# Kernel tuning notes

Hardware: AMD Instinct MI355X
Metric: run time of the kernel (lower is better)

The kernel has to match this reference:

```python
import jax, jax.numpy as jnp
import numpy as np

# dims (must match input_specs / init_kwargs)
T, B_SZ, K, OBS_LAST = 512, 8, 128, 2
OBS_DIM = K * OBS_LAST          # 256
N_ACTIONS = 64
N_UNITS, N_FEAT = 256, 8
D_INNER = N_UNITS * N_FEAT      # 2048
H, N_STATE = 16, 64             # p_heads, state_size
P = D_INNER // H                # headdim = 128


def setup_inputs() -> dict:
    key = jax.random.key(0)
    ks = jax.random.split(key, 12)
    s = lambda fan_in: 1.0 / np.sqrt(fan_in)
    return {
        "obs": jax.random.normal(ks[0], (T, B_SZ, K, OBS_LAST), jnp.float32),
        # input projection obs_dim -> d_inner
        "W_in": jax.random.normal(ks[1], (OBS_DIM, D_INNER), jnp.float32) * s(OBS_DIM),
        "b_in": jnp.zeros((D_INNER,), jnp.float32),
        # SSD cell params (Mamba2-style)
        "A_log": jnp.log(jnp.linspace(1.0, 16.0, H).astype(jnp.float32)),
        "dt_bias": jnp.full((H,), -2.0, jnp.float32),
        "W_dt": jax.random.normal(ks[2], (D_INNER, H), jnp.float32) * s(D_INNER),
        "W_B": jax.random.normal(ks[3], (D_INNER, H * N_STATE), jnp.float32) * s(D_INNER),
        "W_C": jax.random.normal(ks[4], (D_INNER, H * N_STATE), jnp.float32) * s(D_INNER),
        # SSD output projection d_inner -> n_units
        "W_yo": jax.random.normal(ks[5], (D_INNER, N_UNITS), jnp.float32) * s(D_INNER),
        "b_yo": jnp.zeros((N_UNITS,), jnp.float32),
        # policy head n_units -> n_actions
        "W_head": jax.random.normal(ks[6], (N_UNITS, N_ACTIONS), jnp.float32) * s(N_UNITS),
        "b_head": jnp.zeros((N_ACTIONS,), jnp.float32),
    }


def _ssd_scan(x, A_log, dt_bias, W_dt, W_B, W_C):
    # x: (T, B, D_INNER) -> y: (T, B, D_INNER) via selective state-space scan
    t, b, _ = x.shape
    dt = jax.nn.softplus(jnp.einsum("tbd,dh->tbh", x, W_dt) + dt_bias)   # (T,B,H)
    Bm = jnp.einsum("tbd,dm->tbm", x, W_B).reshape(t, b, H, N_STATE)      # (T,B,H,N)
    Cm = jnp.einsum("tbd,dm->tbm", x, W_C).reshape(t, b, H, N_STATE)      # (T,B,H,N)
    xh = x.reshape(t, b, H, P)                                            # (T,B,H,P)
    decay = jnp.exp(-jnp.exp(A_log)[None, None, :] * dt)                  # (T,B,H)

    def step(h, inp):
        dec_t, dt_t, B_t, C_t, x_t = inp
        # h: (B,H,P,N); rank-1 input update per head
        h = dec_t[:, :, None, None] * h + dt_t[:, :, None, None] * jnp.einsum(
            "bhp,bhn->bhpn", x_t, B_t)
        y = jnp.einsum("bhpn,bhn->bhp", h, C_t)                           # (B,H,P)
        return h, y

    h0 = jnp.zeros((b, H, P, N_STATE), x.dtype)
    _, ys = jax.lax.scan(step, h0, (decay, dt, Bm, Cm, xh))
    return ys.reshape(t, b, D_INNER)


def reference(obs, W_in, b_in, A_log, dt_bias, W_dt, W_B, W_C, W_yo, b_yo, W_head, b_head):
    t, b = obs.shape[0], obs.shape[1]
    flat = obs.reshape(t * b, -1)                                 # (t*B, obs_dim)
    x = jax.nn.relu(flat @ W_in + b_in).reshape(t, b, D_INNER)     # (t,B,d_inner)
    y = _ssd_scan(x, A_log, dt_bias, W_dt, W_B, W_C)               # (t,B,d_inner)
    hid = jnp.einsum("tbd,du->tbu", y, W_yo) + b_yo                # (t,B,n_units)
    z = jax.nn.relu(hid).reshape(t * b, N_UNITS)
    logits = z @ W_head + b_head
    return logits.reshape(t, b, N_ACTIONS)
```

## Files before the change

kernel.cpp:

```cpp
#include <hip/hip_runtime.h>
#include <cstdint>
#include <cstddef>

typedef unsigned short u16;
typedef __attribute__((ext_vector_type(8))) __bf16 bf16x8;
typedef __attribute__((ext_vector_type(4))) float floatx4;

#define T_DIM   512
#define B_SZ    8
#define ROWS    4096
#define OBS_D   256
#define D_IN    2048
#define NHEAD   16
#define NSTATE  64
#define PDIM    128
#define NUNITS  256
#define NACT    64
#define NSEG    4
#define SEGT    128
#define SLOT    (B_SZ * NHEAD * PDIM * NSTATE)
#define BCSTR   2176
#define BCN     2048

__host__ __device__ __forceinline__ float bf2f(u16 u) {
    union { uint32_t i; float f; } v; v.i = ((uint32_t)u) << 16; return v.f;
}
__host__ __device__ __forceinline__ u16 f2bf(float f) {
    union { float f; uint32_t i; } v; v.f = f;
    uint32_t r = v.i + 0x7FFFu + ((v.i >> 16) & 1u);
    return (u16)(r >> 16);
}

__device__ __forceinline__ void glds16(const u16* g, u16* l) {
    __builtin_amdgcn_global_load_lds(
        (__attribute__((address_space(1))) void*)g,
        (__attribute__((address_space(3))) void*)l, 16, 0, 0);
}

__global__ __launch_bounds__(256) void ActorAgent_27625229647898_kernel(
        float* __restrict__ out, int n, float v) {
    for (int i = blockIdx.x * 256 + threadIdx.x; i < n; i += gridDim.x * 256)
        out[i] = v;
}

__global__ __launch_bounds__(256) void prep(const float* __restrict__ obs,
                                            const float* __restrict__ W_dt,
                                            const float* __restrict__ W_in,
                                            const float* __restrict__ W_B,
                                            const float* __restrict__ W_C,
                                            const float* __restrict__ W_yo,
                                            const float* __restrict__ W_head,
                                            u16* __restrict__ obsb,
                                            u16* __restrict__ WinT, u16* __restrict__ WBCT,
                                            u16* __restrict__ WdtT,
                                            u16* __restrict__ WyoT, u16* __restrict__ WheadT) {
    int bid = blockIdx.x;
    if (bid < 160) {
        const int NOBS = ROWS * OBS_D;
        const int NDT  = D_IN * NHEAD;
        for (int i = bid * 256 + threadIdx.x; i < NOBS + NDT; i += 160 * 256) {
            if (i < NOBS) obsb[i] = f2bf(obs[i]);
            else {
                int j = i - NOBS;
                int k = j >> 4, n = j & 15;
                WdtT[n * D_IN + k] = f2bf(W_dt[j]);
            }
        }
        return;
    }
    bid -= 160;
    const float* src; u16* dst; int R, C, bx, by;
    if (bid < 512)       { src = W_in;   dst = WinT;   R = 256;  C = 2048; bx = bid & 63; by = bid >> 6; }
    else if (bid < 2560) { int i = bid - 512;  src = W_B;  dst = WBCT; R = 2048; C = 1024; bx = i & 31; by = i >> 5; }
    else if (bid < 4608) { int i = bid - 2560; src = W_C;  dst = WBCT + (size_t)1024 * 2048; R = 2048; C = 1024; bx = i & 31; by = i >> 5; }
    else if (bid < 5120) { int i = bid - 4608; src = W_yo; dst = WyoT; R = 2048; C = 256;  bx = i & 7;  by = i >> 3; }
    else                 { int i = bid - 5120; src = W_head; dst = WheadT; R = 256; C = 64; bx = i & 1; by = i >> 1; }
    __shared__ float t[32][33];
    int c0 = bx * 32, r0 = by * 32;
    int tx = threadIdx.x & 31, ty = threadIdx.x >> 5;
#pragma unroll
    for (int i = 0; i < 32; i += 8)
        t[ty + i][tx] = src[(size_t)(r0 + ty + i) * C + c0 + tx];
    __syncthreads();
#pragma unroll
    for (int i = 0; i < 32; i += 8)
        dst[(size_t)(c0 + ty + i) * R + r0 + tx] = f2bf(t[tx][ty + i]);
}

template <int ACT, int OUT_BF16, int HAS_BIAS>
__global__ __launch_bounds__(256) void gemm_bt128(const u16* __restrict__ A,
                                                  const u16* __restrict__ BT,
                                                  const float* __restrict__ bias,
                                                  void* __restrict__ Cout,
                                                  int M, int N, int K, int ldc) {
    __shared__ __align__(16) u16 sA[2][128 * 64];
    __shared__ __align__(16) u16 sB[2][128 * 64];
    const int tid  = threadIdx.x;
    const int wave = tid >> 6, lane = tid & 63;
    const int quad = lane >> 4, lr = lane & 15;
    const int wm = wave & 1, wn = wave >> 1;
    const int m0 = blockIdx.x * 128, n0 = blockIdx.y * 128;
    const int r0 = wave * 32 + (lane >> 3);
    const int kel = (((lane & 7) ^ ((lane >> 3) & 7))) * 8;
    const int rsw = lr & 7;

    floatx4 acc[4][4];
#pragma unroll
    for (int i = 0; i < 4; i++)
#pragma unroll
        for (int j = 0; j < 4; j++)
#pragma unroll
            for (int r = 0; r < 4; r++) acc[i][j][r] = 0.f;

    const u16* apg = A + (size_t)(m0 + r0) * K + kel;
    const u16* bpg = BT + (size_t)(n0 + r0) * K + kel;
    const int ntk = K >> 6;

#define STAGE128(t, sb) do {                                                   \
        int kk_ = (t) << 6;                                                    \
        _Pragma("unroll")                                                      \
        for (int g = 0; g < 4; ++g) {                                          \
            glds16(apg + (size_t)(g * 8) * K + kk_,                            \
                   &sA[sb][(wave * 32 + g * 8) * 64]);                         \
            glds16(bpg + (size_t)(g * 8) * K + kk_,                            \
                   &sB[sb][(wave * 32 + g * 8) * 64]);                         \
        }                                                                      \
    } while (0)

    STAGE128(0, 0);
    for (int t = 0; t < ntk; ++t) {
        const int s = t & 1;
        asm volatile("s_waitcnt vmcnt(0)" ::: "memory");
        __builtin_amdgcn_s_barrier();
        asm volatile("" ::: "memory");
        if (t + 1 < ntk) STAGE128(t + 1, s ^ 1);
#pragma unroll
        for (int ks = 0; ks < 2; ++ks) {
            bf16x8 af[4], bfr[4];
#pragma unroll
            for (int i = 0; i < 4; i++)
                af[i] = *(const bf16x8*)&sA[s][(wm * 64 + i * 16 + lr) * 64 + ((ks * 4 + quad) ^ rsw) * 8];
#pragma unroll
            for (int j = 0; j < 4; j++)
                bfr[j] = *(const bf16x8*)&sB[s][(wn * 64 + j * 16 + lr) * 64 + ((ks * 4 + quad) ^ rsw) * 8];
#pragma unroll
            for (int i = 0; i < 4; i++)
#pragma unroll
                for (int j = 0; j < 4; j++)
                    acc[i][j] = __builtin_amdgcn_mfma_f32_16x16x32_bf16(af[i], bfr[j], acc[i][j], 0, 0, 0);
        }
        asm volatile("" ::: "memory");
    }
#undef STAGE128
#pragma unroll
    for (int j = 0; j < 4; j++) {
        int col = n0 + wn * 64 + j * 16 + lr;
        float bvv = HAS_BIAS ? bias[col] : 0.f;
#pragma unroll
        for (int i = 0; i < 4; i++) {
#pragma unroll
            for (int r = 0; r < 4; r++) {
                int row = m0 + wm * 64 + i * 16 + quad * 4 + r;
                float v = acc[i][j][r] + bvv;
                if (ACT) v = fmaxf(v, 0.f);
                if (OUT_BF16) ((u16*)Cout)[(size_t)row * ldc + col] = f2bf(v);
                else          ((float*)Cout)[(size_t)row * ldc + col] = v;
            }
        }
    }
}

template <int ACT, int OUT_BF16>
__global__ __launch_bounds__(256) void gemm_bt64(const u16* __restrict__ A,
                                                 const u16* __restrict__ BT,
                                                 const float* __restrict__ bias,
                                                 void* __restrict__ Cout,
                                                 int M, int N, int K) {
    __shared__ __align__(16) u16 sA[4][64 * 64];
    __shared__ __align__(16) u16 sB[4][64 * 64];
    const int tid  = threadIdx.x;
    const int wave = tid >> 6, lane = tid & 63;
    const int quad = lane >> 4, lr = lane & 15;
    const int m0 = blockIdx.x * 64, n0 = blockIdx.y * 64;
    const int srl = lane >> 3;
    const int sc = (((lane & 7) ^ ((lane >> 3) & 7))) * 8;
    const int rsw = lr & 7;

    floatx4 acc[4];
#pragma unroll
    for (int i = 0; i < 4; i++)
#pragma unroll
        for (int j = 0; j < 4; j++) acc[i][j] = 0.f;

    const u16* apg = A + (size_t)(m0 + wave * 16 + srl) * K + sc;
    const u16* bpg = BT + (size_t)(n0 + wave * 16 + srl) * K + sc;
    const int ntk = K >> 6;

#define STAGE64(t, sb) do {                                            \
        int kk_ = (t) << 6;                                            \
        glds16(apg + kk_,                 &sA[sb][(wave * 16) * 64]);  \
        glds16(apg + (size_t)8 * K + kk_, &sA[sb][(wave * 16 + 8) * 64]);\
        glds16(bpg + kk_,                 &sB[sb][(wave * 16) * 64]);  \
        glds16(bpg + (size_t)8 * K + kk_, &sB[sb][(wave * 16 + 8) * 64]);\
    } while (0)

    STAGE64(0, 0);
    STAGE64(1, 1);
    for (int t = 0; t < ntk; ++t) {
        const int s = t & 3;
        if (t + 1 < ntk) {
            asm volatile("s_waitcnt vmcnt(4)" ::: "memory");
        } else {
            asm volatile("s_waitcnt vmcnt(0)" ::: "memory");
        }
        __builtin_amdgcn_s_barrier();
        asm volatile("" ::: "memory");
        __builtin_amdgcn_s_setprio(1);
#pragma unroll
        for (int ks = 0; ks < 2; ++ks) {
            bf16x8 af = *(const bf16x8*)&sA[s][(wave * 16 + lr) * 64 + ((ks * 4 + quad) ^ rsw) * 8];
#pragma unroll
            for (int nt = 0; nt < 4; nt++) {
                bf16x8 bf = *(const bf16x8*)&sB[s][(nt * 16 + lr) * 64 + ((ks * 4 + quad) ^ rsw) * 8];
                acc[nt] = __builtin_amdgcn_mfma_f32_16x16x32_bf16(af, bf, acc[nt], 0, 0, 0);
            }
        }
        __builtin_amdgcn_s_setprio(0);
        asm volatile("" ::: "memory");
        if (t + 2 < ntk) STAGE64(t + 2, (t + 2) & 3);
    }
#undef STAGE64
#pragma unroll
    for (int nt = 0; nt < 4; nt++) {
        int col = n0 + nt * 16 + lr;
        float bvv = bias ? bias[col] : 0.f;
#pragma unroll
        for (int r = 0; r < 4; r++) {
            int row = m0 + wave * 16 + quad * 4 + r;
            float v = acc[nt][r] + bvv;
            if (ACT) v = fmaxf(v, 0.f);
            if (OUT_BF16) ((u16*)Cout)[(size_t)row * N + col] = f2bf(v);
            else          ((float*)Cout)[(size_t)row * N + col] = v;
        }
    }
}

__global__ __launch_bounds__(512) void dtdecay(const u16* __restrict__ xb,
                                               const u16* __restrict__ WdtT,
                                               const float* __restrict__ dt_bias,
                                               const float* __restrict__ A_log,
                                               float* __restrict__ dtv,
                                               float* __restrict__ decayv) {
    __shared__ __align__(16) u16 sw[NHEAD * D_IN];
    const int tid = threadIdx.x;
#pragma unroll
    for (int i = 0; i < 8; ++i) {
        int idx = (tid + i * 512) * 8;
        *(uint4*)&sw[idx] = *(const uint4*)(WdtT + idx);
    }
    __syncthreads();
    const int wave = tid >> 6, lane = tid & 63;
    const int q = lane >> 4, lr = lane & 15;
    const int row0 = blockIdx.x * 16 + wave * 2;
    const u16* xp0 = xb + (size_t)row0 * D_IN;
    const u16* xp1 = xb + (size_t)(row0 + 1) * D_IN;
    float acc0[4] = {0.f, 0.f, 0.f, 0.f};
    float acc1[4] = {0.f, 0.f, 0.f, 0.f};
#pragma unroll 4
    for (int k0 = 0; k0 < 16; ++k0) {
        const int kk = k0 * 128 + lr * 8;
        uint4 xv0 = *(const uint4*)(xp0 + kk);
        uint4 xv1 = *(const uint4*)(xp1 + kk);
        const u16* xu0 = (const u16*)&xv0;
        const u16* xu1 = (const u16*)&xv1;
        float xf0[8], xf1[8];
#pragma unroll
        for (int j = 0; j < 8; ++j) { xf0[j] = bf2f(xu0[j]); xf1[j] = bf2f(xu1[j]); }
#pragma unroll
        for (int j = 0; j < 4; ++j) {
            uint4 wv = *(const uint4*)&sw[(q * 4 + j) * D_IN + kk];
            const u16* wu = (const u16*)&wv;
#pragma unroll
            for (int jj = 0; jj < 8; ++jj) {
                float wf = bf2f(wu[jj]);
                acc0[j] = fmaf(xf0[jj], wf, acc0[j]);
                acc1[j] = fmaf(xf1[jj], wf, acc1[j]);
            }
        }
    }
#pragma unroll
    for (int m = 1; m <= 8; m <<= 1)
#pragma unroll
        for (int j = 0; j < 4; ++j) {
            acc0[j] += __shfl_xor(acc0[j], m);
            acc1[j] += __shfl_xor(acc1[j], m);
        }
    if (lr == 0) {
#pragma unroll
        for (int j = 0; j < 4; ++j) {
            int h = q * 4 + j;
            float ae = expf(A_log[h]);
            float z0 = acc0[j] + dt_bias[h];
            float sp0 = (z0 > 20.f) ? z0 : log1pf(expf(z0));
            float z1 = acc1[j] + dt_bias[h];
            float sp1 = (z1 > 20.f) ? z1 : log1pf(expf(z1));
            dtv[row0 * NHEAD + h] = sp0;
            decayv[row0 * NHEAD + h] = expf(-ae * sp0);
            dtv[(row0 + 1) * NHEAD + h] = sp1;
            decayv[(row0 + 1) * NHEAD + h] = expf(-ae * sp1);
        }
    }
}

__global__ __launch_bounds__(256) void seg_state(const u16* __restrict__ xw,
                                                 const u16* __restrict__ BCm,
                                                 const float* __restrict__ dtv,
                                                 const float* __restrict__ decayv,
                                                 float* __restrict__ Hbuf) {
    const int blk = blockIdx.x;
    const int seg = blk >> 7;
    const int b   = (blk >> 4) & 7;
    const int h   = blk & 15;
    const int tid = threadIdx.x;
    const int pgrp = tid >> 3;
    const int oct  = tid & 7;

    __shared__ __align__(16) u16 sx[SEGT][PDIM];
    __shared__ __align__(16) u16 sbm[SEGT][NSTATE];
    __shared__ float sw[SEGT];
    __shared__ float sdt[SEGT];
    __shared__ float sdec[SEGT];
    __shared__ float sP[32];

    const int t0 = seg * SEGT;

#pragma unroll
    for (int k = 0; k < 8; ++k) {
        int idx = tid + k * 256;
        int t = idx >> 4, c = (idx & 15) * 8;
        int r = (t0 + t) * B_SZ + b;
        *(uint4*)&sx[t][c] = *(const uint4*)(xw + (size_t)r * D_IN + h * PDIM + c);
    }
#pragma unroll
    for (int k = 0; k < 4; ++k) {
        int idx = tid + k * 256;
        int t = idx >> 3, c = (idx & 7) * 8;
        int r = (t0 + t) * B_SZ + b;
        *(uint4*)&sbm[t][c] = *(const uint4*)(BCm + (size_t)r * BCSTR + h * NSTATE + c);
    }
    if (tid < SEGT)            sdt[tid] = dtv[((t0 + tid) * B_SZ + b) * NHEAD + h];
    else if (tid < 2 * SEGT)   sdec[tid - SEGT] = decayv[((t0 + tid - SEGT) * B_SZ + b) * NHEAD + h];
    __syncthreads();

    if (tid < 32) {
        float p = 1.f;
        for (int i = 3; i >= 0; --i) {
            int t = tid * 4 + i;
            sw[t] = sdt[t] * p;
            p *= sdec[t];
        }
        sP[tid] = p;
    }
    __syncthreads();
    if (tid == 0) {
        float suf = 1.f;
        for (int q = 31; q >= 0; --q) { float tmp = sP[q]; sP[q] = suf; suf *= tmp; }
    }
    __syncthreads();
    if (tid < 32) {
        float m = sP[tid];
        for (int i = 0; i < 4; ++i) sw[tid * 4 + i] *= m;
    }
    __syncthreads();

    float acc[4][8];
#pragma unroll
    for (int i = 0; i < 4; i++)
#pragma unroll
        for (int j = 0; j < 8; j++) acc[i][j] = 0.f;

    for (int t = 0; t < SEGT; ++t) {
        float w = sw[t];
        const u16* xp = &sx[t][pgrp * 4];
        const u16* bp = &sbm[t][oct * 8];
        float xv[4], bv[8];
#pragma unroll
        for (int i = 0; i < 4; i++) xv[i] = w * bf2f(xp[i]);
#pragma unroll
        for (int j = 0; j < 8; j++) bv[j] = bf2f(bp[j]);
#pragma unroll
        for (int i = 0; i < 4; i++)
#pragma unroll
            for (int j = 0; j < 8; j++)
                acc[i][j] = fmaf(xv[i], bv[j], acc[i][j]);
    }

    float* base = Hbuf + (size_t)seg * SLOT +
                  (((size_t)b * NHEAD + h) * PDIM + pgrp * 4) * NSTATE + oct * 8;
#pragma unroll
    for (int i = 0; i < 4; i++) {
        *(float4*)(base + (size_t)i * NSTATE)     = make_float4(acc[i][0], acc[i][1], acc[i][2], acc[i][3]);
        *(float4*)(base + (size_t)i * NSTATE + 4) = make_float4(acc[i][4], acc[i][5], acc[i][6], acc[i][7]);
    }
}

__global__ __launch_bounds__(256) void seg_prefix(const float* __restrict__ Hbuf,
                                                  const float* __restrict__ decayv,
                                                  u16* __restrict__ Hbf) {
    const int blk = blockIdx.x;
    const int b  = blk >> 6;
    const int h  = (blk >> 2) & 15;
    const int ec = blk & 3;
    const int tid = threadIdx.x;

    __shared__ float sA[NSEG];

    if (tid < 64 * (NSEG - 2)) {
        int s = 1 + (tid >> 6);
        int i = tid & 63;
        int t = s * SEGT + i * 2;
        float p = decayv[(t * B_SZ + b) * NHEAD + h] *
                  decayv[((t + 1) * B_SZ + b) * NHEAD + h];
        p *= __shfl_xor(p, 1);
        p *= __shfl_xor(p, 2);
        p *= __shfl_xor(p, 4);
        p *= __shfl_xor(p, 8);
        p *= __shfl_xor(p, 16);
        p *= __shfl_xor(p, 32);
        if (i == 0) sA[s] = p;
    }
    __syncthreads();

    const size_t base = (((size_t)b * NHEAD + h) * PDIM * NSTATE) + (size_t)ec * 2048 + tid * 8;
    float4 P0 = *(const float4*)(Hbuf + base);
    float4 P1 = *(const float4*)(Hbuf + base + 4);
    u16 pk[8];
    pk[0] = f2bf(P0.x); pk[1] = f2bf(P0.y); pk[2] = f2bf(P0.z); pk[3] = f2bf(P0.w);
    pk[4] = f2bf(P1.x); pk[5] = f2bf(P1.y); pk[6] = f2bf(P1.z); pk[7] = f2bf(P1.w);
    *(uint4*)(Hbf + base) = *(const uint4*)pk;
#pragma unroll
    for (int s = 1; s <= NSEG - 2; ++s) {
        float a = sA[s];
        const float* slot = Hbuf + (size_t)s * SLOT + base;
        float4 h0 = *(const float4*)(slot);
        float4 h1 = *(const float4*)(slot + 4);
        P0.x = fmaf(a, P0.x, h0.x); P0.y = fmaf(a, P0.y, h0.y);
        P0.z = fmaf(a, P0.z, h0.z); P0.w = fmaf(a, P0.w, h0.w);
        P1.x = fmaf(a, P1.x, h1.x); P1.y = fmaf(a, P1.y, h1.y);
        P1.z = fmaf(a, P1.z, h1.z); P1.w = fmaf(a, P1.w, h1.w);
        pk[0] = f2bf(P0.x); pk[1] = f2bf(P0.y); pk[2] = f2bf(P0.z); pk[3] = f2bf(P0.w);
        pk[4] = f2bf(P1.x); pk[5] = f2bf(P1.y); pk[6] = f2bf(P1.z); pk[7] = f2bf(P1.w);
        *(uint4*)(Hbf + (size_t)s * SLOT + base) = *(const uint4*)pk;
    }
}

__global__ __launch_bounds__(256) void chunk_scan(const u16* __restrict__ BCm,
                                                  const float* __restrict__ dtv,
                                                  const float* __restrict__ decayv,
                                                  const u16* __restrict__ Hbf,
                                                  u16* __restrict__ xb) {
    __shared__ __align__(16) u16 sB_[128][68];
    __shared__ __align__(16) u16 sC_[128][68];
    __shared__ __align__(16) u16 sS[128][132];
    __shared__ __align__(16) u16 sXT[128][36];
    __shared__ float sdt[SEGT], sL[SEGT], sEL[SEGT], stmp[32];

    const int blk = blockIdx.x;
    const int seg = blk >> 7, b = (blk >> 4) & 7, h = blk & 15;
    const int tid = threadIdx.x;
    const int wave = tid >> 6, lane = tid & 63;
    const int quad = lane >> 4, lr = lane & 15;
    const int wm = wave & 1, wn = wave >> 1;
    const int t0 = seg * SEGT;

#pragma unroll
    for (int it = 0; it < 4; ++it) {
        int idx = tid + it * 256;
        int t = idx >> 3, c = (idx & 7) * 8;
        int r = (t0 + t) * B_SZ + b;
        *(uint4*)&sB_[t][c] = *(const uint4*)(BCm + (size_t)r * BCSTR + h * NSTATE + c);
        *(uint4*)&sC_[t][c] = *(const uint4*)(BCm + (size_t)r * BCSTR + 1024 + h * NSTATE + c);
    }
    if (tid < SEGT) sdt[tid] = dtv[((t0 + tid) * B_SZ + b) * NHEAD + h];
    else if (tid < 2 * SEGT) {
        int t = tid - SEGT;
        sL[t] = __logf(fmaxf(decayv[((t0 + t) * B_SZ + b) * NHEAD + h], 1e-30f));
    }
    __syncthreads();
    if (tid < 32) {
        float s = 0.f, v[4];
#pragma unroll
        for (int i = 0; i < 4; ++i) { s += sL[tid * 4 + i]; v[i] = s; }
        stmp[tid] = s;
#pragma unroll
        for (int i = 0; i < 4; ++i) sL[tid * 4 + i] = v[i];
    }
    __syncthreads();
    if (tid == 0) {
        float run = 0.f;
        for (int q = 0; q < 32; ++q) { float c2 = stmp[q]; stmp[q] = run; run += c2; }
    }
    __syncthreads();
    if (tid < 32) {
        float off = stmp[tid];
#pragma unroll
        for (int i = 0; i < 4; ++i) sL[tid * 4 + i] += off;
    }
    __syncthreads();
    if (tid < SEGT) sEL[tid] = __expf(sL[tid]);

    floatx4 accS[4][4];
#pragma unroll
    for (int i = 0; i < 4; i++)
#pragma unroll
        for (int j = 0; j < 4; j++)
#pragma unroll
            for (int r = 0; r < 4; r++) accS[i][j][r] = 0.f;
#pragma unroll
    for (int k0 = 0; k0 < 64; k0 += 32) {
        bf16x8 af[4], bfr[4];
#pragma unroll
        for (int i = 0; i < 4; i++)
            af[i] = *(const bf16x8*)&sB_[wm * 64 + i * 16 + lr][k0 + quad * 8];
#pragma unroll
        for (int j = 0; j < 4; j++)
            bfr[j] = *(const bf16x8*)&sC_[wn * 64 + j * 16 + lr][k0 + quad * 8];
#pragma unroll
        for (int i = 0; i < 4; i++)
#pragma unroll
            for (int j = 0; j < 4; j++)
                accS[i][j] = __builtin_amdgcn_mfma_f32_16x16x32_bf16(af[i], bfr[j], accS[i][j], 0, 0, 0);
    }
#pragma unroll
    for (int j = 0; j < 4; j++) {
        int tt = wn * 64 + j * 16 + lr;
        float Lt = sL[tt];
#pragma unroll
        for (int i = 0; i < 4; i++) {
#pragma unroll
            for (int r = 0; r < 4; r++) {
                int tp = wm * 64 + i * 16 + quad * 4 + r;
                float v = 0.f;
                if (tp <= tt) v = accS[i][j][r] * sdt[tp] * __expf(Lt - sL[tp]);
                sS[tt][tp] = f2bf(v);
            }
        }
    }

    floatx4 acc[4][4];
#pragma unroll
    for (int i = 0; i < 4; i++)
#pragma unroll
        for (int j = 0; j < 4; j++)
#pragma unroll
            for (int r = 0; r < 4; r++) acc[i][j][r] = 0.f;
    __syncthreads();
    if (seg > 0) {
        const u16* hbase = Hbf + (size_t)(seg - 1) * SLOT + (((size_t)b * NHEAD + h) * PDIM) * NSTATE;
#pragma unroll
        for (int k0 = 0; k0 < 64; k0 += 32) {
            bf16x8 af[4], bfr[4];
#pragma unroll
            for (int i = 0; i < 4; i++)
                af[i] = *(const bf16x8*)&sC_[wm * 64 + i * 16 + lr][k0 + quad * 8];
#pragma unroll
            for (int j = 0; j < 4; j++)
                bfr[j] = *(const bf16x8*)(hbase + (size_t)(wn * 64 + j * 16 + lr) * NSTATE + k0 + quad * 8);
#pragma unroll
            for (int i = 0; i < 4; i++)
#pragma unroll
                for (int j = 0; j < 4; j++)
                    acc[i][j] = __builtin_amdgcn_mfma_f32_16x16x32_bf16(af[i], bfr[j], acc[i][j], 0, 0, 0);
        }
#pragma unroll
        for (int i = 0; i < 4; i++) {
#pragma unroll
            for (int r = 0; r < 4; r++) {
                float el = sEL[wm * 64 + i * 16 + quad * 4 + r];
#pragma unroll
                for (int j = 0; j < 4; j++) acc[i][j][r] *= el;
            }
        }
    }

    const int px = tid & 127, koh = (tid >> 7) * 16;
    for (int kc = 0; kc < 128; kc += 32) {
        u16 xv[16];
#pragma unroll
        for (int j2 = 0; j2 < 16; ++j2) {
            int tp = kc + koh + j2;
            xv[j2] = xb[(size_t)((t0 + tp) * B_SZ + b) * D_IN + h * PDIM + px];
        }
        __syncthreads();
        *(uint4*)&sXT[px][koh]     = *(const uint4*)&xv[0];
        *(uint4*)&sXT[px][koh + 8] = *(const uint4*)&xv[8];
        __syncthreads();
        bf16x8 af[4], bfr[4];
#pragma unroll
        for (int i = 0; i < 4; i++)
            af[i] = *(const bf16x8*)&sS[wm * 64 + i * 16 + lr][kc + quad * 8];
#pragma unroll
        for (int j = 0; j < 4; j++)
            bfr[j] = *(const bf16x8*)&sXT[wn * 64 + j * 16 + lr][quad * 8];
#pragma unroll
        for (int i = 0; i < 4; i++)
#pragma unroll
            for (int j = 0; j < 4; j++)
                acc[i][j] = __builtin_amdgcn_mfma_f32_16x16x32_bf16(af[i], bfr[j], acc[i][j], 0, 0, 0);
    }

#pragma unroll
    for (int j = 0; j < 4; j++) {
        int p = wn * 64 + j * 16 + lr;
#pragma unroll
        for (int i = 0; i < 4; i++) {
#pragma unroll
            for (int r = 0; r < 4; r++) {
                int t = wm * 64 + i * 16 + quad * 4 + r;
                xb[(size_t)((t0 + t) * B_SZ + b) * D_IN + h * PDIM + p] = f2bf(acc[i][j][r]);
            }
        }
    }
}

extern "C" void kernel_launch(void* const* d_in, const int* in_sizes, int n_in,
                              void* d_out, int out_size, void* d_ws, size_t ws_size,
                              hipStream_t stream) {
    const float* obs     = (const float*)d_in[0];
    const float* W_in    = (const float*)d_in[1];
    const float* b_in    = (const float*)d_in[2];
    const float* A_log   = (const float*)d_in[3];
    const float* dt_bias = (const float*)d_in[4];
    const float* W_dt    = (const float*)d_in[5];
    const float* W_B     = (const float*)d_in[6];
    const float* W_C     = (const float*)d_in[7];
    const float* W_yo    = (const float*)d_in[8];
    const float* b_yo    = (const float*)d_in[9];
    const float* W_head  = (const float*)d_in[10];
    const float* b_head  = (const float*)d_in[11];

    char* ws = (char*)d_ws;
    size_t o = 0;
    u16*   xb     = (u16*)(ws + o);   o += (size_t)ROWS * D_IN * 2;
    u16*   BCm    = (u16*)(ws + o);   o += (size_t)ROWS * BCSTR * 2;
    float* dtv    = (float*)(ws + o); o += (size_t)ROWS * NHEAD * 4;
    float* decayv = (float*)(ws + o); o += (size_t)ROWS * NHEAD * 4;
    u16*   zb     = (u16*)(ws + o);   o += (size_t)ROWS * NUNITS * 2;
    float* Hseg   = (float*)(ws + o); o += (size_t)(NSEG - 1) * SLOT * 4;
    u16*   Hbf    = (u16*)(ws + o);   o += (size_t)(NSEG - 1) * SLOT * 2;
    u16*   obsb   = (u16*)(ws + o);   o += (size_t)ROWS * OBS_D * 2;
    u16*   WinT   = (u16*)(ws + o);   o += (size_t)D_IN * OBS_D * 2;
    u16*   WBCT   = (u16*)(ws + o);   o += (size_t)BCN * D_IN * 2;
    u16*   WdtT   = (u16*)(ws + o);   o += (size_t)NHEAD * D_IN * 2;
    u16*   WyoT   = (u16*)(ws + o);   o += (size_t)NUNITS * D_IN * 2;
    u16*   WheadT = (u16*)(ws + o);   o += (size_t)NACT * NUNITS * 2;

    ActorAgent_27625229647898_kernel<<<dim3(1), 256, 0, stream>>>((float*)d_out, 0, 0.f);

    prep<<<dim3(160 + 5136), 256, 0, stream>>>(obs, W_dt, W_in, W_B, W_C, W_yo, W_head,
                                               obsb, WinT, WBCT, WdtT, WyoT, WheadT);

    gemm_bt128<1, 1, 1><<<dim3(32, 16), 256, 0, stream>>>(obsb, WinT, b_in, xb, ROWS, D_IN, OBS_D, D_IN);
    dtdecay<<<dim3(256), 512, 0, stream>>>(xb, WdtT, dt_bias, A_log, dtv, decayv);
    gemm_bt128<0, 1, 0><<<dim3(32, 16), 256, 0, stream>>>(xb, WBCT, (const float*)nullptr, BCm, ROWS, BCN, D_IN, BCSTR);
    seg_state<<<dim3((NSEG - 1) * 128), 256, 0, stream>>>(xb, BCm, dtv, decayv, Hseg);
    seg_prefix<<<dim3(512), 256, 0, stream>>>(Hseg, decayv, Hbf);
    chunk_scan<<<dim3(NSEG * 128), 256, 0, stream>>>(BCm, dtv, decayv, Hbf, xb);
    gemm_bt64<1, 1><<<dim3(64, 4), 256, 0, stream>>>(xb, WyoT, b_yo, zb, ROWS, NUNITS, D_IN);
    gemm_bt64<0, 0><<<dim3(64, 1), 256, 0, stream>>>(zb, WheadT, b_head, (float*)d_out, ROWS, NACT, NUNITS);
}
```

Baseline: 232.7 us.

## Move segment-state outer product to MFMA and deepen GEMM K-tile to 128

```diff
diff --git a/kernel.cpp b/kernel.cpp
--- a/kernel.cpp
+++ b/kernel.cpp
@@ -36,6 +36,9 @@
         (__attribute__((address_space(1))) void*)g,
         (__attribute__((address_space(3))) void*)l, 16, 0, 0);
 }
+
+#define LBAR() do { asm volatile("s_waitcnt lgkmcnt(0)" ::: "memory"); \
+                    __builtin_amdgcn_s_barrier(); } while (0)
 
 __global__ __launch_bounds__(256) void ActorAgent_27625229647898_kernel(
         float* __restrict__ out, int n, float v) {
@@ -176,15 +179,14 @@
                                                  const float* __restrict__ bias,
                                                  void* __restrict__ Cout,
                                                  int M, int N, int K) {
-    __shared__ __align__(16) u16 sA[4][64 * 64];
-    __shared__ __align__(16) u16 sB[4][64 * 64];
+    __shared__ __align__(16) u16 sA[2][64 * 128];
+    __shared__ __align__(16) u16 sB[2][64 * 128];
     const int tid  = threadIdx.x;
     const int wave = tid >> 6, lane = tid & 63;
     const int quad = lane >> 4, lr = lane & 15;
     const int m0 = blockIdx.x * 64, n0 = blockIdx.y * 64;
-    const int srl = lane >> 3;
-    const int sc = (((lane & 7) ^ ((lane >> 3) & 7))) * 8;
-    const int rsw = lr & 7;
+    const int rl = lane >> 4;
+    const int cl = lane & 15;
 
     floatx4 acc[4];
 #pragma unroll
@@ -192,42 +194,44 @@
 #pragma unroll
         for (int j = 0; j < 4; j++) acc[i][j] = 0.f;
 
-    const u16* apg = A + (size_t)(m0 + wave * 16 + srl) * K + sc;
-    const u16* bpg = BT + (size_t)(n0 + wave * 16 + srl) * K + sc;
-    const int ntk = K >> 6;
-
-#define STAGE64(t, sb) do {                                            \
-        int kk_ = (t) << 6;                                            \
-        glds16(apg + kk_,                 &sA[sb][(wave * 16) * 64]);  \
-        glds16(apg + (size_t)8 * K + kk_, &sA[sb][(wave * 16 + 8) * 64]);\
-        glds16(bpg + kk_,                 &sB[sb][(wave * 16) * 64]);  \
-        glds16(bpg + (size_t)8 * K + kk_, &sB[sb][(wave * 16 + 8) * 64]);\
+    size_t aoff[4], boff[4];
+#pragma unroll
+    for (int g = 0; g < 4; ++g) {
+        int ro = g * 4 + rl;
+        int ch = cl ^ ro;
+        aoff[g] = (size_t)(m0 + wave * 16 + ro) * K + (size_t)ch * 8;
+        boff[g] = (size_t)(n0 + wave * 16 + ro) * K + (size_t)ch * 8;
+    }
+    const int ntk = K >> 7;
+
+#define STAGE64(t, sb) do {                                                    \
+        int kk_ = (t) << 7;                                                    \
+        _Pragma("unroll")                                                      \
+        for (int g = 0; g < 4; ++g) {                                          \
+            glds16(A + aoff[g] + kk_,  &sA[sb][(wave * 16 + g * 4) * 128]);    \
+            glds16(BT + boff[g] + kk_, &sB[sb][(wave * 16 + g * 4) * 128]);    \
+        }                                                                      \
     } while (0)
 
     STAGE64(0, 0);
-    STAGE64(1, 1);
     for (int t = 0; t < ntk; ++t) {
-        const int s = t & 3;
-        if (t + 1 < ntk) {
-            asm volatile("s_waitcnt vmcnt(4)" ::: "memory");
-        } else {
-            asm volatile("s_waitcnt vmcnt(0)" ::: "memory");
-        }
+        const int s = t & 1;
+        asm volatile("s_waitcnt vmcnt(0)" ::: "memory");
         __builtin_amdgcn_s_barrier();
         asm volatile("" ::: "memory");
+        if (t + 1 < ntk) STAGE64(t + 1, s ^ 1);
         __builtin_amdgcn_s_setprio(1);
 #pragma unroll
-        for (int ks = 0; ks < 2; ++ks) {
-            bf16x8 af = *(const bf16x8*)&sA[s][(wave * 16 + lr) * 64 + ((ks * 4 + quad) ^ rsw) * 8];
+        for (int ks = 0; ks < 4; ++ks) {
+            bf16x8 af = *(const bf16x8*)&sA[s][(wave * 16 + lr) * 128 + ((ks * 4 + quad) ^ lr) * 8];
 #pragma unroll
             for (int nt = 0; nt < 4; nt++) {
-                bf16x8 bf = *(const bf16x8*)&sB[s][(nt * 16 + lr) * 64 + ((ks * 4 + quad) ^ rsw) * 8];
+                bf16x8 bf = *(const bf16x8*)&sB[s][(nt * 16 + lr) * 128 + ((ks * 4 + quad) ^ lr) * 8];
                 acc[nt] = __builtin_amdgcn_mfma_f32_16x16x32_bf16(af, bf, acc[nt], 0, 0, 0);
             }
         }
         __builtin_amdgcn_s_setprio(0);
         asm volatile("" ::: "memory");
-        if (t + 2 < ntk) STAGE64(t + 2, (t + 2) & 3);
     }
 #undef STAGE64
 #pragma unroll
@@ -322,85 +326,114 @@
     const int b   = (blk >> 4) & 7;
     const int h   = blk & 15;
     const int tid = threadIdx.x;
-    const int pgrp = tid >> 3;
-    const int oct  = tid & 7;
-
-    __shared__ __align__(16) u16 sx[SEGT][PDIM];
-    __shared__ __align__(16) u16 sbm[SEGT][NSTATE];
-    __shared__ float sw[SEGT];
-    __shared__ float sdt[SEGT];
-    __shared__ float sdec[SEGT];
-    __shared__ float sP[32];
+    const int wave = tid >> 6, lane = tid & 63;
+    const int quad = lane >> 4, lr = lane & 15;
+    const int wm = wave & 1, wn = wave >> 1;
+
+    __shared__ __align__(16) u16 sxw[PDIM][SEGT + 4];
+    __shared__ __align__(16) u16 sbT[NSTATE][SEGT + 6];
+    __shared__ float sw_[SEGT], sdt[SEGT], sdec[SEGT], sP[32];
 
     const int t0 = seg * SEGT;
 
+    uint4 xv4[8];
 #pragma unroll
     for (int k = 0; k < 8; ++k) {
         int idx = tid + k * 256;
         int t = idx >> 4, c = (idx & 15) * 8;
         int r = (t0 + t) * B_SZ + b;
-        *(uint4*)&sx[t][c] = *(const uint4*)(xw + (size_t)r * D_IN + h * PDIM + c);
-    }
+        xv4[k] = *(const uint4*)(xw + (size_t)r * D_IN + h * PDIM + c);
+    }
+    uint4 bv4[4];
 #pragma unroll
     for (int k = 0; k < 4; ++k) {
         int idx = tid + k * 256;
         int t = idx >> 3, c = (idx & 7) * 8;
         int r = (t0 + t) * B_SZ + b;
-        *(uint4*)&sbm[t][c] = *(const uint4*)(BCm + (size_t)r * BCSTR + h * NSTATE + c);
-    }
+        bv4[k] = *(const uint4*)(BCm + (size_t)r * BCSTR + h * NSTATE + c);
+    }
+
     if (tid < SEGT)            sdt[tid] = dtv[((t0 + tid) * B_SZ + b) * NHEAD + h];
     else if (tid < 2 * SEGT)   sdec[tid - SEGT] = decayv[((t0 + tid - SEGT) * B_SZ + b) * NHEAD + h];
-    __syncthreads();
+    LBAR();
 
     if (tid < 32) {
         float p = 1.f;
         for (int i = 3; i >= 0; --i) {
             int t = tid * 4 + i;
-            sw[t] = sdt[t] * p;
+            sw_[t] = sdt[t] * p;
             p *= sdec[t];
         }
         sP[tid] = p;
     }
-    __syncthreads();
+    LBAR();
     if (tid == 0) {
         float suf = 1.f;
         for (int q = 31; q >= 0; --q) { float tmp = sP[q]; sP[q] = suf; suf *= tmp; }
     }
-    __syncthreads();
+    LBAR();
     if (tid < 32) {
         float m = sP[tid];
-        for (int i = 0; i < 4; ++i) sw[tid * 4 + i] *= m;
-    }
-    __syncthreads();
-
-    float acc[4][8];
+        for (int i = 0; i < 4; ++i) sw_[tid * 4 + i] *= m;
+    }
+    LBAR();
+
+#pragma unroll
+    for (int k = 0; k < 8; ++k) {
+        int idx = tid + k * 256;
+        int t = idx >> 4, c = (idx & 15) * 8;
+        float w = sw_[t];
+        const u16* u = (const u16*)&xv4[k];
+#pragma unroll
+        for (int j = 0; j < 8; ++j)
+            sxw[c + j][t] = f2bf(bf2f(u[j]) * w);
+    }
+#pragma unroll
+    for (int k = 0; k < 4; ++k) {
+        int idx = tid + k * 256;
+        int t = idx >> 3, c = (idx & 7) * 8;
+        const u16* u = (const u16*)&bv4[k];
+#pragma unroll
+        for (int j = 0; j < 8; ++j)
+            sbT[c + j][t] = u[j];
+    }
+    LBAR();
+
+    floatx4 acc[4][2];
 #pragma unroll
     for (int i = 0; i < 4; i++)
 #pragma unroll
-        for (int j = 0; j < 8; j++) acc[i][j] = 0.f;
-
-    for (int t = 0; t < SEGT; ++t) {
-        float w = sw[t];
-        const u16* xp = &sx[t][pgrp * 4];
-        const u16* bp = &sbm[t][oct * 8];
-        float xv[4], bv[8];
-#pragma unroll
-        for (int i = 0; i < 4; i++) xv[i] = w * bf2f(xp[i]);
-#pragma unroll
-        for (int j = 0; j < 8; j++) bv[j] = bf2f(bp[j]);
+        for (int j = 0; j < 2; j++)
+#pragma unroll
+            for (int r = 0; r < 4; r++) acc[i][j][r] = 0.f;
+#pragma unroll
+    for (int kk = 0; kk < 128; kk += 32) {
+        bf16x8 af[4], bfr[2];
 #pragma unroll
         for (int i = 0; i < 4; i++)
-#pragma unroll
-            for (int j = 0; j < 8; j++)
-                acc[i][j] = fmaf(xv[i], bv[j], acc[i][j]);
-    }
-
-    float* base = Hbuf + (size_t)seg * SLOT +
-                  (((size_t)b * NHEAD + h) * PDIM + pgrp * 4) * NSTATE + oct * 8;
+            af[i] = *(const bf16x8*)&sxw[wm * 64 + i * 16 + lr][kk + quad * 8];
+#pragma unroll
+        for (int j = 0; j < 2; j++)
+            bfr[j] = *(const bf16x8*)&sbT[wn * 32 + j * 16 + lr][kk + quad * 8];
+#pragma unroll
+        for (int i = 0; i < 4; i++)
+#pragma unroll
+            for (int j = 0; j < 2; j++)
+                acc[i][j] = __builtin_amdgcn_mfma_f32_16x16x32_bf16(af[i], bfr[j], acc[i][j], 0, 0, 0);
+    }
+
+    float* base = Hbuf + (size_t)seg * SLOT + (((size_t)b * NHEAD + h) * PDIM) * NSTATE;
 #pragma unroll
     for (int i = 0; i < 4; i++) {
-        *(float4*)(base + (size_t)i * NSTATE)     = make_float4(acc[i][0], acc[i][1], acc[i][2], acc[i][3]);
-        *(float4*)(base + (size_t)i * NSTATE + 4) = make_float4(acc[i][4], acc[i][5], acc[i][6], acc[i][7]);
+#pragma unroll
+        for (int j = 0; j < 2; j++) {
+            int n = wn * 32 + j * 16 + lr;
+#pragma unroll
+            for (int r = 0; r < 4; r++) {
+                int p = wm * 64 + i * 16 + quad * 4 + r;
+                base[(size_t)p * NSTATE + n] = acc[i][j][r];
+            }
+        }
     }
 }
 
```

Result: faster. 218.8 us (-6.0%).
